# Kernel optimization log

Hardware: AMD Instinct MI355X
Metric: run time of the kernel (lower is better)

## Reference

```python
import jax, jax.numpy as jnp
import numpy as np

N, D, H, E, K = 8192, 1024, 2048, 8, 2

def setup_inputs() -> dict:
    key = jax.random.key(0)
    ks = jax.random.split(key, 8)
    x = jax.random.normal(ks[0], (N, D), dtype=jnp.float32)
    # Expert params stacked over the expert axis (E, ...)
    W1 = jax.random.normal(ks[1], (E, D, H), dtype=jnp.float32) * (1.0 / np.sqrt(D))
    b1 = jnp.zeros((E, H), dtype=jnp.float32)
    W2 = jax.random.normal(ks[2], (E, H, D), dtype=jnp.float32) * (1.0 / np.sqrt(H))
    b2 = jnp.zeros((E, D), dtype=jnp.float32)
    # Gating linear
    Wg = jax.random.normal(ks[3], (D, E), dtype=jnp.float32) * (1.0 / np.sqrt(D))
    bg = jnp.zeros((E,), dtype=jnp.float32)
    # Externalized gating noise (torch uses randn_like(logits) * 0.1)
    noise = jax.random.normal(ks[4], (N, E), dtype=jnp.float32)
    return {"x": x, "W1": W1, "b1": b1, "W2": W2, "b2": b2, "Wg": Wg, "bg": bg, "noise": noise}


def reference(x, W1, b1, W2, b2, Wg, bg, noise):
    n = x.shape[0]
    # --- gating: noisy top-k + softmax over top-k, scattered to dense weights ---
    logits = x @ Wg + bg                                  # [N, E]
    noisy = logits + 0.1 * noise
    top_v, top_i = jax.lax.top_k(noisy, K)                # [N, K]
    w = jax.nn.softmax(top_v, axis=-1)                    # [N, K]
    rows = jnp.arange(n)[:, None]
    sparse_w = jnp.zeros_like(logits).at[rows, top_i].set(w)  # [N, E]
    # --- all experts on all tokens (faithful to the dense-stack implementation) ---
    h = jax.nn.relu(jnp.einsum('nd,edh->neh', x, W1) + b1)    # [N, E, H]
    expert_out = jnp.einsum('neh,ehd->ned', h, W2) + b2       # [N, E, D]
    # --- weighted combine ---
    return jnp.einsum('ne,ned->nd', sparse_w, expert_out)     # [N, D]
```

## Files before the change

kernel.cpp:

```cpp
#include <hip/hip_runtime.h>
#include <stdint.h>
#include <stddef.h>

#define NTOK 8192
#define DDIM 1024
#define HDIM 2048
#define NEXP 8

typedef __attribute__((ext_vector_type(8))) short short8;
typedef __attribute__((ext_vector_type(8))) unsigned short ushort8;
typedef __attribute__((ext_vector_type(4))) float floatx4;

#define AS1 __attribute__((address_space(1)))
#define AS3 __attribute__((address_space(3)))

#define MAXRT 136
#define MAXT1 (MAXRT * (HDIM / 128))
#define MAXT2 (MAXRT * (DDIM / 128))

constexpr size_t OFF_CNT  = 0;
constexpr size_t OFF_TB1  = 256;
constexpr size_t OFF_TB2  = OFF_TB1 + 8960;
constexpr size_t OFF_TKI  = OFF_TB2 + 4608;
constexpr size_t OFF_TKW  = OFF_TKI + (size_t)NTOK * 8;
constexpr size_t OFF_LIST = OFF_TKW + (size_t)NTOK * 8;
constexpr size_t OFF_WTS  = OFF_LIST + (size_t)NEXP * NTOK * 4;
constexpr size_t OFF_XBF  = OFF_WTS + (size_t)NEXP * NTOK * 4;
constexpr size_t OFF_W1T  = OFF_XBF + (size_t)NTOK * DDIM * 2;
constexpr size_t OFF_W2T  = OFF_W1T + (size_t)NEXP * DDIM * HDIM * 2;
constexpr size_t OFF_H    = OFF_W2T + (size_t)NEXP * DDIM * HDIM * 2;

__device__ __forceinline__ unsigned short f2bf(float f) {
  union { float f; unsigned u; } v; v.f = f;
  unsigned r = v.u + 0x7FFFu + ((v.u >> 16) & 1u);
  return (unsigned short)(r >> 16);
}

__global__ __launch_bounds__(256) void gate_kernel(
    const float* __restrict__ x, const float* __restrict__ Wg,
    const float* __restrict__ bg, const float* __restrict__ noise,
    int2* __restrict__ tki, float2* __restrict__ tkw,
    unsigned short* __restrict__ xbf) {
  int lane = threadIdx.x & 63;
  int wid  = threadIdx.x >> 6;
  int token = blockIdx.x * 4 + wid;
  const float* xr = x + (size_t)token * DDIM;
  unsigned short* xo = xbf + (size_t)token * DDIM;
  double acc[NEXP];
#pragma unroll
  for (int e = 0; e < NEXP; ++e) acc[e] = 0.0;
  for (int d = lane; d < DDIM; d += 64) {
    float xv = xr[d];
    xo[d] = f2bf(xv);
    const floatx4* wp = (const floatx4*)(Wg + d * NEXP);
    floatx4 w0 = wp[0], w1 = wp[1];
#pragma unroll
    for (int j = 0; j < 4; ++j) {
      acc[j]     += (double)xv * (double)w0[j];
      acc[4 + j] += (double)xv * (double)w1[j];
    }
  }
#pragma unroll
  for (int e = 0; e < NEXP; ++e)
#pragma unroll
    for (int off = 32; off > 0; off >>= 1) acc[e] += __shfl_xor(acc[e], off);
  if (lane == 0) {
    float nv[NEXP];
#pragma unroll
    for (int e = 0; e < NEXP; ++e) {
      float lg = (float)(acc[e] + (double)bg[e]);
      nv[e] = lg + 0.1f * noise[token * NEXP + e];
    }
    int i1 = 0; float v1 = nv[0];
#pragma unroll
    for (int e = 1; e < NEXP; ++e) if (nv[e] > v1) { v1 = nv[e]; i1 = e; }
    int i2 = -1; float v2 = -3.4e38f;
#pragma unroll
    for (int e = 0; e < NEXP; ++e) if (e != i1 && nv[e] > v2) { v2 = nv[e]; i2 = e; }
    float tt  = expf(v2 - v1);
    tki[token] = make_int2(i1, i2);
    tkw[token] = make_float2(1.0f / (1.0f + tt), tt / (1.0f + tt));
  }
}

__global__ __launch_bounds__(256) void scatter_kernel(
    const int2* __restrict__ tki, const float2* __restrict__ tkw,
    int* __restrict__ counts, int* __restrict__ lists, float* __restrict__ wts) {
  int e = blockIdx.x;
  int tid = threadIdx.x;
  int lane = tid & 63, wid = tid >> 6;
  __shared__ int wave_cnt[4];
  __shared__ int run_total;
  if (tid == 0) run_total = 0;
  __syncthreads();
  for (int t0 = 0; t0 < NTOK; t0 += 256) {
    int tok = t0 + tid;
    int2 ki = tki[tok];
    float2 kw = tkw[tok];
    bool sel = (ki.x == e) || (ki.y == e);
    float w = (ki.x == e) ? kw.x : kw.y;
    unsigned long long mask = __ballot(sel);
    int pos = __popcll(mask & ((1ull << lane) - 1ull));
    if (lane == 0) wave_cnt[wid] = __popcll(mask);
    __syncthreads();
    int base = run_total;
    for (int i = 0; i < wid; ++i) base += wave_cnt[i];
    if (sel) {
      lists[e * NTOK + base + pos] = tok;
      wts[e * NTOK + base + pos] = w;
    }
    __syncthreads();
    if (tid == 0) run_total += wave_cnt[0] + wave_cnt[1] + wave_cnt[2] + wave_cnt[3];
    __syncthreads();
  }
  if (tid == 0) counts[e] = run_total;
}

__global__ __launch_bounds__(256) void build_tiles_kernel(
    const int* __restrict__ counts, int* __restrict__ tb1, int* __restrict__ tb2) {
  int tid = threadIdx.x;
  int ct[8], cum[9];
  cum[0] = 0;
#pragma unroll
  for (int e = 0; e < 8; ++e) { ct[e] = (counts[e] + 127) >> 7; cum[e + 1] = cum[e] + ct[e]; }
  int nt = cum[8];
  constexpr int NBY1 = HDIM / 128, NBY2 = DDIM / 128;
  if (tid == 0) { tb1[0] = nt * NBY1; tb2[0] = nt * NBY2; }
  for (int idx = tid; idx < nt * NBY1; idx += 256) {
    int e = 0;
    while (idx >= cum[e + 1] * NBY1) ++e;
    int r = idx - cum[e] * NBY1;
    int by = r / ct[e], bx = r - by * ct[e];
    tb1[1 + idx] = (e << 16) | (bx << 8) | by;
  }
  for (int idx = tid; idx < nt * NBY2; idx += 256) {
    int e = 0;
    while (idx >= cum[e + 1] * NBY2) ++e;
    int r = idx - cum[e] * NBY2;
    int by = r / ct[e], bx = r - by * ct[e];
    tb2[1 + idx] = (e << 16) | (bx << 8) | by;
  }
}

__global__ __launch_bounds__(256) void transpose_cvt_kernel(
    const float* __restrict__ W, unsigned short* __restrict__ WT, int R, int C) {
  __shared__ float tile[64][65];
  int e = blockIdx.z;
  const float* Win = W + (size_t)e * R * C;
  unsigned short* Wout = WT + (size_t)e * R * C;
  int c0 = blockIdx.x * 64, r0 = blockIdx.y * 64;
  int tx = threadIdx.x & 63, ty = threadIdx.x >> 6;
#pragma unroll
  for (int i = ty; i < 64; i += 4)
    tile[i][tx] = Win[(size_t)(r0 + i) * C + c0 + tx];
  __syncthreads();
  int cc = threadIdx.x >> 2, seg = (threadIdx.x & 3) * 16;
  ushort8 o0, o1;
#pragma unroll
  for (int j = 0; j < 8; ++j) o0[j] = f2bf(tile[seg + j][cc]);
#pragma unroll
  for (int j = 0; j < 8; ++j) o1[j] = f2bf(tile[seg + 8 + j][cc]);
  unsigned short* outp = Wout + (size_t)(c0 + cc) * R + r0 + seg;
  *(ushort8*)(outp) = o0;
  *(ushort8*)(outp + 8) = o1;
}

template <int KDIM, int NDIM, bool IS_G1>
__global__ __launch_bounds__(256) void moe_gemm_kernel(
    const unsigned short* __restrict__ Abase,
    const unsigned short* __restrict__ Bbase,
    const float* __restrict__ bias,
    const int* __restrict__ counts, const int* __restrict__ lists,
    const float* __restrict__ wts, const int* __restrict__ tbl,
    unsigned short* __restrict__ Hout, float* __restrict__ Out) {
  __shared__ __align__(16) char smem[32768];
  constexpr int NT = KDIM / 32;

  int ntiles = tbl[0];
  if ((int)blockIdx.x >= ntiles) return;
  int desc = tbl[1 + blockIdx.x];
  int e  = desc >> 16;
  int bx = (desc >> 8) & 0xff;
  int by = desc & 0xff;

  int Me, off_e = 0;
  {
    int c[8];
#pragma unroll
    for (int i = 0; i < 8; ++i) c[i] = counts[i];
    Me = c[e];
#pragma unroll
    for (int i = 0; i < 8; ++i) if (i < e) off_e += c[i];
  }

  int tid = threadIdx.x;
  int lane = tid & 63, wid = tid >> 6;
  int wr = wid >> 1, wc = wid & 1;
  int r16 = lane & 15, g4 = lane >> 4;

  int r0 = tid >> 2;
  int ch = ((tid & 3) ^ ((r0 >> 1) & 3)) * 8;
  const unsigned short *sA0, *sA1, *sB0, *sB1;
  {
    int lr0 = bx * 128 + r0, lr1 = lr0 + 64;
    if (IS_G1) {
      int tk0 = lists[e * NTOK + (lr0 < Me ? lr0 : 0)];
      int tk1 = lists[e * NTOK + (lr1 < Me ? lr1 : 0)];
      sA0 = Abase + (size_t)tk0 * KDIM + ch;
      sA1 = Abase + (size_t)tk1 * KDIM + ch;
    } else {
      sA0 = Abase + (size_t)(off_e + (lr0 < Me ? lr0 : 0)) * KDIM + ch;
      sA1 = Abase + (size_t)(off_e + (lr1 < Me ? lr1 : 0)) * KDIM + ch;
    }
    sB0 = Bbase + ((size_t)e * NDIM + by * 128 + r0) * KDIM + ch;
    sB1 = sB0 + (size_t)64 * KDIM;
  }

  auto stage = [&](int t) {
    int buf = t & 1;
    size_t ko = (size_t)t * 32;
    char* da = smem + buf * 8192 + tid * 16;
    char* db = smem + 16384 + buf * 8192 + tid * 16;
    __builtin_amdgcn_global_load_lds((const AS1 void*)(sA0 + ko), (AS3 void*)da, 16, 0, 0);
    __builtin_amdgcn_global_load_lds((const AS1 void*)(sA1 + ko), (AS3 void*)(da + 4096), 16, 0, 0);
    __builtin_amdgcn_global_load_lds((const AS1 void*)(sB0 + ko), (AS3 void*)db, 16, 0, 0);
    __builtin_amdgcn_global_load_lds((const AS1 void*)(sB1 + ko), (AS3 void*)(db + 4096), 16, 0, 0);
  };

  int aoff[4], boff[4];
#pragma unroll
  for (int m = 0; m < 4; ++m) {
    int rowa = wr * 64 + m * 16 + r16;
    aoff[m] = rowa * 64 + ((g4 ^ ((rowa >> 1) & 3)) * 16);
  }
#pragma unroll
  for (int n = 0; n < 4; ++n) {
    int rowb = wc * 64 + n * 16 + r16;
    boff[n] = 16384 + rowb * 64 + ((g4 ^ ((rowb >> 1) & 3)) * 16);
  }

  floatx4 acc[4][4];
#pragma unroll
  for (int m = 0; m < 4; ++m)
#pragma unroll
    for (int n = 0; n < 4; ++n) acc[m][n] = (floatx4){0.f, 0.f, 0.f, 0.f};

  stage(0);
  stage(1);

  for (int t = 0; t < NT; ++t) {
    if (t + 1 < NT) { asm volatile("s_waitcnt vmcnt(4)" ::: "memory"); }
    else            { asm volatile("s_waitcnt vmcnt(0)" ::: "memory"); }
    __builtin_amdgcn_s_barrier();
    __builtin_amdgcn_sched_barrier(0);
    const char* pa = smem + (t & 1) * 8192;
    const char* pb = smem + (t & 1) * 8192;
    short8 a[4], b[4];
#pragma unroll
    for (int m = 0; m < 4; ++m) a[m] = *(const short8*)(pa + aoff[m]);
#pragma unroll
    for (int n = 0; n < 4; ++n) b[n] = *(const short8*)(pb + boff[n]);
    __builtin_amdgcn_s_setprio(1);
#pragma unroll
    for (int m = 0; m < 4; ++m)
#pragma unroll
      for (int n = 0; n < 4; ++n)
        acc[m][n] = __builtin_amdgcn_mfma_f32_16x16x32_bf16(a[m], b[n], acc[m][n], 0, 0, 0);
    __builtin_amdgcn_s_setprio(0);
    __builtin_amdgcn_s_barrier();
    __builtin_amdgcn_sched_barrier(0);
    if (t + 2 < NT) stage(t + 2);
  }

  if constexpr (IS_G1) {
#pragma unroll
    for (int m = 0; m < 4; ++m) {
#pragma unroll
      for (int i = 0; i < 4; ++i) {
        int lrow = bx * 128 + wr * 64 + m * 16 + g4 * 4 + i;
        if (lrow < Me) {
          size_t hbase = (size_t)(off_e + lrow) * NDIM + by * 128;
#pragma unroll
          for (int n = 0; n < 4; ++n) {
            int col = wc * 64 + n * 16 + r16;
            float v = acc[m][n][i] + bias[e * NDIM + by * 128 + col];
            Hout[hbase + col] = f2bf(fmaxf(v, 0.f));
          }
        }
      }
    }
  } else {
#pragma unroll
    for (int m = 0; m < 4; ++m) {
#pragma unroll
      for (int i = 0; i < 4; ++i) {
        int lrow = bx * 128 + wr * 64 + m * 16 + g4 * 4 + i;
        if (lrow < Me) {
          int tok = lists[e * NTOK + lrow];
          float w = wts[e * NTOK + lrow];
          float* orow = Out + (size_t)tok * NDIM + by * 128;
#pragma unroll
          for (int n = 0; n < 4; ++n) {
            int col = wc * 64 + n * 16 + r16;
            float v = acc[m][n][i] + bias[e * NDIM + by * 128 + col];
            atomicAdd(orow + col, w * v);
          }
        }
      }
    }
  }
}

extern "C" void kernel_launch(void* const* d_in, const int* in_sizes, int n_in,
                              void* d_out, int out_size, void* d_ws, size_t ws_size,
                              hipStream_t stream) {
  (void)in_sizes; (void)n_in; (void)ws_size;
  const float* x     = (const float*)d_in[0];
  const float* W1    = (const float*)d_in[1];
  const float* b1    = (const float*)d_in[2];
  const float* W2    = (const float*)d_in[3];
  const float* b2    = (const float*)d_in[4];
  const float* Wg    = (const float*)d_in[5];
  const float* bg    = (const float*)d_in[6];
  const float* noise = (const float*)d_in[7];
  float* out = (float*)d_out;

  char* ws = (char*)d_ws;
  int*            counts = (int*)(ws + OFF_CNT);
  int*            tb1    = (int*)(ws + OFF_TB1);
  int*            tb2    = (int*)(ws + OFF_TB2);
  int2*           tki    = (int2*)(ws + OFF_TKI);
  float2*         tkw    = (float2*)(ws + OFF_TKW);
  int*            lists  = (int*)(ws + OFF_LIST);
  float*          wts    = (float*)(ws + OFF_WTS);
  unsigned short* xbf    = (unsigned short*)(ws + OFF_XBF);
  unsigned short* w1t    = (unsigned short*)(ws + OFF_W1T);
  unsigned short* w2t    = (unsigned short*)(ws + OFF_W2T);
  unsigned short* h      = (unsigned short*)(ws + OFF_H);

  hipMemsetAsync(d_out, 0, (size_t)out_size * sizeof(float), stream);
  hipMemsetAsync(counts, 0, 256, stream);

  gate_kernel<<<NTOK / 4, 256, 0, stream>>>(x, Wg, bg, noise, tki, tkw, xbf);
  scatter_kernel<<<NEXP, 256, 0, stream>>>(tki, tkw, counts, lists, wts);
  build_tiles_kernel<<<1, 256, 0, stream>>>(counts, tb1, tb2);
  transpose_cvt_kernel<<<dim3(HDIM / 64, DDIM / 64, NEXP), 256, 0, stream>>>(W1, w1t, DDIM, HDIM);
  transpose_cvt_kernel<<<dim3(DDIM / 64, HDIM / 64, NEXP), 256, 0, stream>>>(W2, w2t, HDIM, DDIM);

  moe_gemm_kernel<DDIM, HDIM, true>
      <<<MAXT1, 256, 0, stream>>>(xbf, w1t, b1, counts, lists, wts, tb1, h, nullptr);
  moe_gemm_kernel<HDIM, DDIM, false>
      <<<MAXT2, 256, 0, stream>>>(h, w2t, b2, counts, lists, wts, tb2, nullptr, out);
}
```

Measured before the change: 383.1 us.

## Store GEMM operands in K-blocked layout and remap tiles per XCD

Adds a gather kernel that copies routed token rows into a contiguous K-blocked [K/32][rows][32] bf16 buffer. The weight transpose and the first GEMM's H output now use the same K-blocked layout, so each stage's loads read one contiguous chunk instead of strided rows. Tile descriptors are also remapped so consecutive work items land on the same XCD, which should improve L2 reuse. The cost is an extra gather pass over activations, and H stores become scattered 2-byte writes.

```diff
diff --git a/kernel.cpp b/kernel.cpp
--- a/kernel.cpp
+++ b/kernel.cpp
@@ -6,6 +6,7 @@
 #define DDIM 1024
 #define HDIM 2048
 #define NEXP 8
+#define GROWS 16384
 
 typedef __attribute__((ext_vector_type(8))) short short8;
 typedef __attribute__((ext_vector_type(8))) unsigned short ushort8;
@@ -26,9 +27,10 @@
 constexpr size_t OFF_LIST = OFF_TKW + (size_t)NTOK * 8;
 constexpr size_t OFF_WTS  = OFF_LIST + (size_t)NEXP * NTOK * 4;
 constexpr size_t OFF_XBF  = OFF_WTS + (size_t)NEXP * NTOK * 4;
-constexpr size_t OFF_W1T  = OFF_XBF + (size_t)NTOK * DDIM * 2;
-constexpr size_t OFF_W2T  = OFF_W1T + (size_t)NEXP * DDIM * HDIM * 2;
-constexpr size_t OFF_H    = OFF_W2T + (size_t)NEXP * DDIM * HDIM * 2;
+constexpr size_t OFF_AKB  = OFF_XBF + (size_t)NTOK * DDIM * 2;
+constexpr size_t OFF_W1KB = OFF_AKB + (size_t)GROWS * DDIM * 2;
+constexpr size_t OFF_W2KB = OFF_W1KB + (size_t)NEXP * DDIM * HDIM * 2;
+constexpr size_t OFF_HKB  = OFF_W2KB + (size_t)NEXP * DDIM * HDIM * 2;
 
 __device__ __forceinline__ unsigned short f2bf(float f) {
   union { float f; unsigned u; } v; v.f = f;
@@ -116,6 +118,24 @@
   if (tid == 0) counts[e] = run_total;
 }
 
+__global__ __launch_bounds__(256) void gather_a_kernel(
+    const unsigned short* __restrict__ xbf, const int* __restrict__ counts,
+    const int* __restrict__ lists, unsigned short* __restrict__ akb) {
+  int kt   = blockIdx.y;
+  int grow = blockIdx.x * 256 + threadIdx.x;
+  int c[8];
+#pragma unroll
+  for (int i = 0; i < 8; ++i) c[i] = counts[i];
+  int e = 0, off = 0;
+#pragma unroll
+  for (int i = 0; i < 8; ++i)
+    if (e == i && grow >= off + c[i]) { off += c[i]; e = i + 1; }
+  int tok = lists[e * NTOK + (grow - off)];
+  const ushort8* s = (const ushort8*)(xbf + (size_t)tok * DDIM + kt * 32);
+  ushort8* d = (ushort8*)(akb + (size_t)kt * GROWS * 32 + (size_t)grow * 32);
+  d[0] = s[0]; d[1] = s[1]; d[2] = s[2]; d[3] = s[3];
+}
+
 __global__ __launch_bounds__(256) void build_tiles_kernel(
     const int* __restrict__ counts, int* __restrict__ tb1, int* __restrict__ tb2) {
   int tid = threadIdx.x;
@@ -160,25 +180,34 @@
   for (int j = 0; j < 8; ++j) o0[j] = f2bf(tile[seg + j][cc]);
 #pragma unroll
   for (int j = 0; j < 8; ++j) o1[j] = f2bf(tile[seg + 8 + j][cc]);
-  unsigned short* outp = Wout + (size_t)(c0 + cc) * R + r0 + seg;
+  int koff = r0 + seg;
+  unsigned short* outp = Wout + (size_t)(koff >> 5) * C * 32
+                              + (size_t)(c0 + cc) * 32 + (koff & 31);
   *(ushort8*)(outp) = o0;
   *(ushort8*)(outp + 8) = o1;
 }
 
 template <int KDIM, int NDIM, bool IS_G1>
 __global__ __launch_bounds__(256) void moe_gemm_kernel(
-    const unsigned short* __restrict__ Abase,
-    const unsigned short* __restrict__ Bbase,
+    const unsigned short* __restrict__ Akb,
+    const unsigned short* __restrict__ Bkb,
     const float* __restrict__ bias,
     const int* __restrict__ counts, const int* __restrict__ lists,
     const float* __restrict__ wts, const int* __restrict__ tbl,
-    unsigned short* __restrict__ Hout, float* __restrict__ Out) {
+    unsigned short* __restrict__ Hkb,
+    float* __restrict__ Out) {
   __shared__ __align__(16) char smem[32768];
   constexpr int NT = KDIM / 32;
+  constexpr size_t A_KT = (size_t)GROWS * 32;
+  constexpr size_t B_KT = (size_t)NDIM * 32;
 
   int ntiles = tbl[0];
-  if ((int)blockIdx.x >= ntiles) return;
-  int desc = tbl[1 + blockIdx.x];
+  int bid = blockIdx.x;
+  if (bid >= ntiles) return;
+  int q = ntiles >> 3, rr = ntiles & 7;
+  int xcd = bid & 7, within = bid >> 3;
+  int widx = (xcd < rr ? xcd * (q + 1) : rr * (q + 1) + (xcd - rr) * q) + within;
+  int desc = tbl[1 + widx];
   int e  = desc >> 16;
   int bx = (desc >> 8) & 0xff;
   int by = desc & 0xff;
@@ -203,28 +232,24 @@
   const unsigned short *sA0, *sA1, *sB0, *sB1;
   {
     int lr0 = bx * 128 + r0, lr1 = lr0 + 64;
-    if (IS_G1) {
-      int tk0 = lists[e * NTOK + (lr0 < Me ? lr0 : 0)];
-      int tk1 = lists[e * NTOK + (lr1 < Me ? lr1 : 0)];
-      sA0 = Abase + (size_t)tk0 * KDIM + ch;
-      sA1 = Abase + (size_t)tk1 * KDIM + ch;
-    } else {
-      sA0 = Abase + (size_t)(off_e + (lr0 < Me ? lr0 : 0)) * KDIM + ch;
-      sA1 = Abase + (size_t)(off_e + (lr1 < Me ? lr1 : 0)) * KDIM + ch;
-    }
-    sB0 = Bbase + ((size_t)e * NDIM + by * 128 + r0) * KDIM + ch;
-    sB1 = sB0 + (size_t)64 * KDIM;
+    int g0 = off_e + (lr0 < Me ? lr0 : 0);
+    int g1 = off_e + (lr1 < Me ? lr1 : 0);
+    sA0 = Akb + (size_t)g0 * 32 + ch;
+    sA1 = Akb + (size_t)g1 * 32 + ch;
+    const unsigned short* be = Bkb + (size_t)e * KDIM * NDIM;
+    sB0 = be + (size_t)(by * 128 + r0) * 32 + ch;
+    sB1 = be + (size_t)(by * 128 + 64 + r0) * 32 + ch;
   }
 
   auto stage = [&](int t) {
     int buf = t & 1;
-    size_t ko = (size_t)t * 32;
     char* da = smem + buf * 8192 + tid * 16;
     char* db = smem + 16384 + buf * 8192 + tid * 16;
-    __builtin_amdgcn_global_load_lds((const AS1 void*)(sA0 + ko), (AS3 void*)da, 16, 0, 0);
-    __builtin_amdgcn_global_load_lds((const AS1 void*)(sA1 + ko), (AS3 void*)(da + 4096), 16, 0, 0);
-    __builtin_amdgcn_global_load_lds((const AS1 void*)(sB0 + ko), (AS3 void*)db, 16, 0, 0);
-    __builtin_amdgcn_global_load_lds((const AS1 void*)(sB1 + ko), (AS3 void*)(db + 4096), 16, 0, 0);
+    size_t ao = (size_t)t * A_KT, bo = (size_t)t * B_KT;
+    __builtin_amdgcn_global_load_lds((const AS1 void*)(sA0 + ao), (AS3 void*)da, 16, 0, 0);
+    __builtin_amdgcn_global_load_lds((const AS1 void*)(sA1 + ao), (AS3 void*)(da + 4096), 16, 0, 0);
+    __builtin_amdgcn_global_load_lds((const AS1 void*)(sB0 + bo), (AS3 void*)db, 16, 0, 0);
+    __builtin_amdgcn_global_load_lds((const AS1 void*)(sB1 + bo), (AS3 void*)(db + 4096), 16, 0, 0);
   };
 
   int aoff[4], boff[4];
@@ -279,12 +304,12 @@
       for (int i = 0; i < 4; ++i) {
         int lrow = bx * 128 + wr * 64 + m * 16 + g4 * 4 + i;
         if (lrow < Me) {
-          size_t hbase = (size_t)(off_e + lrow) * NDIM + by * 128;
+          size_t grow = (size_t)(off_e + lrow);
 #pragma unroll
           for (int n = 0; n < 4; ++n) {
-            int col = wc * 64 + n * 16 + r16;
-            float v = acc[m][n][i] + bias[e * NDIM + by * 128 + col];
-            Hout[hbase + col] = f2bf(fmaxf(v, 0.f));
+            int col = by * 128 + wc * 64 + n * 16 + r16;
+            float v = acc[m][n][i] + bias[e * NDIM + col];
+            Hkb[(size_t)(col >> 5) * A_KT + grow * 32 + (col & 31)] = f2bf(fmaxf(v, 0.f));
           }
         }
       }
@@ -334,9 +359,10 @@
   int*            lists  = (int*)(ws + OFF_LIST);
   float*          wts    = (float*)(ws + OFF_WTS);
   unsigned short* xbf    = (unsigned short*)(ws + OFF_XBF);
-  unsigned short* w1t    = (unsigned short*)(ws + OFF_W1T);
-  unsigned short* w2t    = (unsigned short*)(ws + OFF_W2T);
-  unsigned short* h      = (unsigned short*)(ws + OFF_H);
+  unsigned short* akb    = (unsigned short*)(ws + OFF_AKB);
+  unsigned short* w1kb   = (unsigned short*)(ws + OFF_W1KB);
+  unsigned short* w2kb   = (unsigned short*)(ws + OFF_W2KB);
+  unsigned short* hkb    = (unsigned short*)(ws + OFF_HKB);
 
   hipMemsetAsync(d_out, 0, (size_t)out_size * sizeof(float), stream);
   hipMemsetAsync(counts, 0, 256, stream);
@@ -344,11 +370,12 @@
   gate_kernel<<<NTOK / 4, 256, 0, stream>>>(x, Wg, bg, noise, tki, tkw, xbf);
   scatter_kernel<<<NEXP, 256, 0, stream>>>(tki, tkw, counts, lists, wts);
   build_tiles_kernel<<<1, 256, 0, stream>>>(counts, tb1, tb2);
-  transpose_cvt_kernel<<<dim3(HDIM / 64, DDIM / 64, NEXP), 256, 0, stream>>>(W1, w1t, DDIM, HDIM);
-  transpose_cvt_kernel<<<dim3(DDIM / 64, HDIM / 64, NEXP), 256, 0, stream>>>(W2, w2t, HDIM, DDIM);
+  gather_a_kernel<<<dim3(GROWS / 256, DDIM / 32), 256, 0, stream>>>(xbf, counts, lists, akb);
+  transpose_cvt_kernel<<<dim3(HDIM / 64, DDIM / 64, NEXP), 256, 0, stream>>>(W1, w1kb, DDIM, HDIM);
+  transpose_cvt_kernel<<<dim3(DDIM / 64, HDIM / 64, NEXP), 256, 0, stream>>>(W2, w2kb, HDIM, DDIM);
 
   moe_gemm_kernel<DDIM, HDIM, true>
-      <<<MAXT1, 256, 0, stream>>>(xbf, w1t, b1, counts, lists, wts, tb1, h, nullptr);
+      <<<MAXT1, 256, 0, stream>>>(akb, w1kb, b1, counts, lists, wts, tb1, hkb, nullptr);
   moe_gemm_kernel<HDIM, DDIM, false>
-      <<<MAXT2, 256, 0, stream>>>(h, w2t, b2, counts, lists, wts, tb2, nullptr, out);
-}
+      <<<MAXT2, 256, 0, stream>>>(hkb, w2kb, b2, counts, lists, wts, tb2, nullptr, out);
+}
```

Result: faster. 367.2 us (-4.2%).
